# Kernel optimization log

Measured on AMD Instinct MI355X. Metric: run time of the kernel, lower is better.

Reference implementation:

```python
import jax, jax.numpy as jnp
import numpy as np

EMB = 128
HID = 512
B = 8192
W = 128


def setup_inputs() -> dict:
    key = jax.random.key(0)
    k1, k2, k3, k4, k5, k6, k7 = jax.random.split(key, 7)
    context_info = jax.random.normal(k1, (B, 4 * HID), dtype=jnp.float32)
    window = jax.random.normal(k2, (B, W, EMB), dtype=jnp.float32)
    window_mask = jax.random.bernoulli(k3, 0.9, (B, W))
    # guarantee at least one valid position per row (center is always valid)
    window_mask = window_mask.at[:, W // 2].set(True)
    ctr = jax.random.normal(k4, (B, EMB), dtype=jnp.float32)
    # learned params
    W_bilinear = jax.random.normal(k5, (EMB, EMB), dtype=jnp.float32) / np.sqrt(EMB)  # nn.Bilinear weight [1, emb, emb] squeezed
    W_linear = jax.random.normal(k6, (1, 4 * HID + EMB), dtype=jnp.float32) / np.sqrt(4 * HID + EMB)
    b_linear = jax.random.normal(k7, (1,), dtype=jnp.float32) * 0.01
    return {"context_info": context_info, "window": window, "window_mask": window_mask,
            "ctr": ctr, "W_bilinear": W_bilinear, "W_linear": W_linear, "b_linear": b_linear}


def reference(context_info, window, window_mask, ctr, W_bilinear, W_linear, b_linear):
    # bilinear attention score: ctr^T W window_t  -> [B, W]
    e = jnp.einsum('be,ef,bwf->bw', ctr, W_bilinear, window)
    invalid = jnp.logical_not(window_mask)
    e = jnp.where(invalid, -jnp.inf, e)
    # subtract per-row max (masked_fill of the broadcast max to 0 at invalid slots)
    m = jnp.max(e, axis=1, keepdims=True)            # [B, 1]
    e = e - jnp.where(invalid, 0.0, m)               # broadcast to [B, W]
    at_weights = jax.nn.softmax(e, axis=1)
    at_weights = jnp.where(invalid, 0.0, at_weights)
    # weighted sum over window -> [B, emb]
    context_eos = jnp.einsum('bw,bwe->be', at_weights, window)
    context_full = jnp.concatenate([context_info, context_eos], axis=1)
    logits = context_full @ W_linear.T + b_linear    # [B, 1]
    return logits
```

## Files before the change

kernel.cpp:

```cpp
#include <hip/hip_runtime.h>

#define EMB  128
#define HID4 2048
#define WIN  128

__global__ __launch_bounds__(256) void eos_fused_kernel(
    const float* __restrict__ ci,
    const float* __restrict__ window,
    const unsigned char* __restrict__ mask_raw,
    const float* __restrict__ ctr,
    const float* __restrict__ Wb,
    const float* __restrict__ WL,
    const float* __restrict__ bL,
    float* __restrict__ out)
{
    const int b    = blockIdx.x;
    const int tid  = threadIdx.x;
    const int lane = tid & 63;
    const int wave = tid >> 6;

    __shared__ float ctr_s[EMB];
    __shared__ float pu_s[2][EMB];
    __shared__ float u_s[EMB];
    __shared__ float acc_s[8][EMB];
    __shared__ float mz_s[8][2];
    __shared__ float red_s[4];
    __shared__ unsigned long long det_s[4][2];
    __shared__ int mode_s;

    {
        const unsigned int* mw = (const unsigned int*)mask_raw;
        int hi = 0, nf = 0;
        if (tid < 128) {
            unsigned int v = mw[tid];
            hi = (v & 0xFFFFFF00u) ? 1 : 0;
            nf = (v != 0u && v != 0x3F800000u) ? 1 : 0;
        }
        unsigned long long bh = __ballot(hi);
        unsigned long long bf = __ballot(nf);
        if (lane == 0) { det_s[wave][0] = bh; det_s[wave][1] = bf; }
    }
    if (tid < EMB) ctr_s[tid] = ctr[(size_t)b * EMB + tid];
    __syncthreads();
    if (tid == 0) {
        unsigned long long ah = det_s[0][0] | det_s[1][0] | det_s[2][0] | det_s[3][0];
        unsigned long long af = det_s[0][1] | det_s[1][1] | det_s[2][1] | det_s[3][1];
        mode_s = (af == 0ULL) ? 2 : (ah ? 0 : 1);
    }

    {
        const int f  = tid & (EMB - 1);
        const int h  = tid >> 7;
        const int e0 = h * 64;
        float s = 0.f;
        #pragma unroll 8
        for (int e = 0; e < 64; ++e)
            s = fmaf(ctr_s[e0 + e], Wb[(e0 + e) * EMB + f], s);
        pu_s[h][f] = s;
    }
    __syncthreads();
    if (tid < EMB) u_s[tid] = pu_s[0][tid] + pu_s[1][tid];
    __syncthreads();

    const int mode = mode_s;
    const int hl   = lane & 31;
    const int hw   = wave * 2 + (lane >> 5);
    float4 u4;
    u4.x = u_s[hl*4+0]; u4.y = u_s[hl*4+1]; u4.z = u_s[hl*4+2]; u4.w = u_s[hl*4+3];

    const float4*        win4 = (const float4*)(window + (size_t)b * WIN * EMB);
    const unsigned char* m8   = mask_raw + (size_t)b * WIN;
    const int*           m32  = (const int*)mask_raw + (size_t)b * WIN;
    const float*         mf   = (const float*)mask_raw + (size_t)b * WIN;

    float  m_run = -1e30f, Z = 0.f;
    float4 acc = make_float4(0.f, 0.f, 0.f, 0.f);

    #pragma unroll 4
    for (int i = 0; i < 16; ++i) {
        const int w = i * 8 + hw;
        float4 wv = win4[w * 32 + hl];
        bool valid;
        if (mode == 0)      valid = (m8[w]  != 0);
        else if (mode == 1) valid = (m32[w] != 0);
        else                valid = (mf[w]  != 0.0f);
        float s = wv.x * u4.x;
        s = fmaf(wv.y, u4.y, s);
        s = fmaf(wv.z, u4.z, s);
        s = fmaf(wv.w, u4.w, s);
        s += __shfl_xor(s, 1);
        s += __shfl_xor(s, 2);
        s += __shfl_xor(s, 4);
        s += __shfl_xor(s, 8);
        s += __shfl_xor(s, 16);
        const float m_new = valid ? fmaxf(m_run, s) : m_run;
        const float scale = __expf(m_run - m_new);
        const float p     = valid ? __expf(s - m_new) : 0.f;
        Z = fmaf(Z, scale, p);
        acc.x = fmaf(acc.x, scale, p * wv.x);
        acc.y = fmaf(acc.y, scale, p * wv.y);
        acc.z = fmaf(acc.z, scale, p * wv.z);
        acc.w = fmaf(acc.w, scale, p * wv.w);
        m_run = m_new;
    }

    acc_s[hw][hl*4+0] = acc.x;
    acc_s[hw][hl*4+1] = acc.y;
    acc_s[hw][hl*4+2] = acc.z;
    acc_s[hw][hl*4+3] = acc.w;
    if (hl == 0) { mz_s[hw][0] = m_run; mz_s[hw][1] = Z; }
    __syncthreads();

    float ce = 0.f;
    if (tid < EMB) {
        float M = mz_s[0][0];
        #pragma unroll
        for (int p = 1; p < 8; ++p) M = fmaxf(M, mz_s[p][0]);
        float Zt = 0.f, a = 0.f;
        #pragma unroll
        for (int p = 0; p < 8; ++p) {
            const float sc = __expf(mz_s[p][0] - M);
            Zt = fmaf(mz_s[p][1], sc, Zt);
            a  = fmaf(acc_s[p][tid], sc, a);
        }
        ce = a / Zt;
    }
    __syncthreads();
    if (tid < EMB) u_s[tid] = ce;
    __syncthreads();

    const float4* ci4 = (const float4*)(ci + (size_t)b * HID4);
    const float4* wl4 = (const float4*)WL;
    float part;
    {
        float4 c0 = ci4[tid],       w0 = wl4[tid];
        float4 c1 = ci4[tid + 256], w1 = wl4[tid + 256];
        part = c0.x * w0.x;
        part = fmaf(c0.y, w0.y, part);
        part = fmaf(c0.z, w0.z, part);
        part = fmaf(c0.w, w0.w, part);
        part = fmaf(c1.x, w1.x, part);
        part = fmaf(c1.y, w1.y, part);
        part = fmaf(c1.z, w1.z, part);
        part = fmaf(c1.w, w1.w, part);
    }
    if (tid < EMB) part = fmaf(u_s[tid], WL[HID4 + tid], part);

    part += __shfl_xor(part, 1);
    part += __shfl_xor(part, 2);
    part += __shfl_xor(part, 4);
    part += __shfl_xor(part, 8);
    part += __shfl_xor(part, 16);
    part += __shfl_xor(part, 32);
    if (lane == 0) red_s[wave] = part;
    __syncthreads();
    if (tid == 0)
        out[b] = red_s[0] + red_s[1] + red_s[2] + red_s[3] + bL[0];
}

extern "C" void kernel_launch(void* const* d_in, const int* in_sizes, int n_in,
                              void* d_out, int out_size, void* d_ws, size_t ws_size,
                              hipStream_t stream) {
    const float*         ci     = (const float*)d_in[0];
    const float*         window = (const float*)d_in[1];
    const unsigned char* mask   = (const unsigned char*)d_in[2];
    const float*         ctr    = (const float*)d_in[3];
    const float*         Wb     = (const float*)d_in[4];
    const float*         WL     = (const float*)d_in[5];
    const float*         bL     = (const float*)d_in[6];
    float*               out    = (float*)d_out;

    const int B = in_sizes[0] / HID4;
    hipLaunchKernelGGL(eos_fused_kernel, dim3(B), dim3(256), 0, stream,
                       ci, window, mask, ctr, Wb, WL, bL, out);
}
```

Before: 125.2 us.

## Preload window rows into registers and replace online softmax with two-pass

All 16 float4 window values per thread and the context_info/W_linear operands are loaded at kernel start, so the long global loads overlap the mask detection and the ctr·W_bilinear projection. The per-thread online softmax with rescaling is replaced by storing scores to shared memory, a block-wide max and sum reduction, then a plain weighted accumulation using the register-resident window. This removes the serial exp/rescale chain and the dependent load-use stalls, but raises register pressure (64 floats of window per thread) and adds extra barriers.

```diff
diff --git a/kernel.cpp b/kernel.cpp
--- a/kernel.cpp
+++ b/kernel.cpp
@@ -18,15 +18,30 @@
     const int tid  = threadIdx.x;
     const int lane = tid & 63;
     const int wave = tid >> 6;
+    const int hl   = lane & 31;
+    const int hw   = wave * 2 + (lane >> 5);
 
     __shared__ float ctr_s[EMB];
     __shared__ float pu_s[2][EMB];
     __shared__ float u_s[EMB];
+    __shared__ float s_s[WIN];
+    __shared__ float p_s[WIN];
     __shared__ float acc_s[8][EMB];
-    __shared__ float mz_s[8][2];
     __shared__ float red_s[4];
+    __shared__ float zinv_s;
     __shared__ unsigned long long det_s[4][2];
     __shared__ int mode_s;
+
+    const float4* win4 = (const float4*)(window + (size_t)b * WIN * EMB);
+    float4 wv[16];
+    #pragma unroll
+    for (int i = 0; i < 16; ++i)
+        wv[i] = win4[(i * 8 + hw) * 32 + hl];
+
+    const float4* ci4 = (const float4*)(ci + (size_t)b * HID4);
+    const float4* wl4 = (const float4*)WL;
+    float4 c0 = ci4[tid], c1 = ci4[tid + 256];
+    float4 w0 = wl4[tid], w1 = wl4[tid + 256];
 
     {
         const unsigned int* mw = (const unsigned int*)mask_raw;
@@ -48,6 +63,16 @@
         mode_s = (af == 0ULL) ? 2 : (ah ? 0 : 1);
     }
 
+    float part;
+    part = c0.x * w0.x;
+    part = fmaf(c0.y, w0.y, part);
+    part = fmaf(c0.z, w0.z, part);
+    part = fmaf(c0.w, w0.w, part);
+    part = fmaf(c1.x, w1.x, part);
+    part = fmaf(c1.y, w1.y, part);
+    part = fmaf(c1.z, w1.z, part);
+    part = fmaf(c1.w, w1.w, part);
+
     {
         const int f  = tid & (EMB - 1);
         const int h  = tid >> 7;
@@ -62,90 +87,80 @@
     if (tid < EMB) u_s[tid] = pu_s[0][tid] + pu_s[1][tid];
     __syncthreads();
 
-    const int mode = mode_s;
-    const int hl   = lane & 31;
-    const int hw   = wave * 2 + (lane >> 5);
     float4 u4;
     u4.x = u_s[hl*4+0]; u4.y = u_s[hl*4+1]; u4.z = u_s[hl*4+2]; u4.w = u_s[hl*4+3];
 
-    const float4*        win4 = (const float4*)(window + (size_t)b * WIN * EMB);
-    const unsigned char* m8   = mask_raw + (size_t)b * WIN;
-    const int*           m32  = (const int*)mask_raw + (size_t)b * WIN;
-    const float*         mf   = (const float*)mask_raw + (size_t)b * WIN;
-
-    float  m_run = -1e30f, Z = 0.f;
-    float4 acc = make_float4(0.f, 0.f, 0.f, 0.f);
-
-    #pragma unroll 4
+    #pragma unroll
     for (int i = 0; i < 16; ++i) {
-        const int w = i * 8 + hw;
-        float4 wv = win4[w * 32 + hl];
-        bool valid;
-        if (mode == 0)      valid = (m8[w]  != 0);
-        else if (mode == 1) valid = (m32[w] != 0);
-        else                valid = (mf[w]  != 0.0f);
-        float s = wv.x * u4.x;
-        s = fmaf(wv.y, u4.y, s);
-        s = fmaf(wv.z, u4.z, s);
-        s = fmaf(wv.w, u4.w, s);
+        float s = wv[i].x * u4.x;
+        s = fmaf(wv[i].y, u4.y, s);
+        s = fmaf(wv[i].z, u4.z, s);
+        s = fmaf(wv[i].w, u4.w, s);
         s += __shfl_xor(s, 1);
         s += __shfl_xor(s, 2);
         s += __shfl_xor(s, 4);
         s += __shfl_xor(s, 8);
         s += __shfl_xor(s, 16);
-        const float m_new = valid ? fmaxf(m_run, s) : m_run;
-        const float scale = __expf(m_run - m_new);
-        const float p     = valid ? __expf(s - m_new) : 0.f;
-        Z = fmaf(Z, scale, p);
-        acc.x = fmaf(acc.x, scale, p * wv.x);
-        acc.y = fmaf(acc.y, scale, p * wv.y);
-        acc.z = fmaf(acc.z, scale, p * wv.z);
-        acc.w = fmaf(acc.w, scale, p * wv.w);
-        m_run = m_new;
+        if (hl == 0) s_s[i * 8 + hw] = s;
     }
-
-    acc_s[hw][hl*4+0] = acc.x;
-    acc_s[hw][hl*4+1] = acc.y;
-    acc_s[hw][hl*4+2] = acc.z;
-    acc_s[hw][hl*4+3] = acc.w;
-    if (hl == 0) { mz_s[hw][0] = m_run; mz_s[hw][1] = Z; }
     __syncthreads();
 
-    float ce = 0.f;
-    if (tid < EMB) {
-        float M = mz_s[0][0];
-        #pragma unroll
-        for (int p = 1; p < 8; ++p) M = fmaxf(M, mz_s[p][0]);
-        float Zt = 0.f, a = 0.f;
-        #pragma unroll
-        for (int p = 0; p < 8; ++p) {
-            const float sc = __expf(mz_s[p][0] - M);
-            Zt = fmaf(mz_s[p][1], sc, Zt);
-            a  = fmaf(acc_s[p][tid], sc, a);
-        }
-        ce = a / Zt;
+    const int mode = mode_s;
+    bool  valid = false;
+    float sc    = 0.f;
+    if (tid < WIN) {
+        if (mode == 0)      valid = (mask_raw[(size_t)b * WIN + tid] != 0);
+        else if (mode == 1) valid = (((const int*)mask_raw)[(size_t)b * WIN + tid] != 0);
+        else                valid = (((const float*)mask_raw)[(size_t)b * WIN + tid] != 0.f);
+        sc = s_s[tid];
+        float sv = valid ? sc : -1e30f;
+        sv = fmaxf(sv, __shfl_xor(sv, 1));
+        sv = fmaxf(sv, __shfl_xor(sv, 2));
+        sv = fmaxf(sv, __shfl_xor(sv, 4));
+        sv = fmaxf(sv, __shfl_xor(sv, 8));
+        sv = fmaxf(sv, __shfl_xor(sv, 16));
+        sv = fmaxf(sv, __shfl_xor(sv, 32));
+        if (lane == 0) red_s[wave] = sv;
     }
     __syncthreads();
-    if (tid < EMB) u_s[tid] = ce;
+    if (tid < WIN) {
+        const float M = fmaxf(red_s[0], red_s[1]);
+        const float p = valid ? __expf(sc - M) : 0.f;
+        p_s[tid] = p;
+        float z = p;
+        z += __shfl_xor(z, 1);
+        z += __shfl_xor(z, 2);
+        z += __shfl_xor(z, 4);
+        z += __shfl_xor(z, 8);
+        z += __shfl_xor(z, 16);
+        z += __shfl_xor(z, 32);
+        if (lane == 0) red_s[2 + wave] = z;
+    }
+    __syncthreads();
+    if (tid == 0) zinv_s = 1.f / (red_s[2] + red_s[3]);
+
+    float4 a4 = make_float4(0.f, 0.f, 0.f, 0.f);
+    #pragma unroll
+    for (int i = 0; i < 16; ++i) {
+        const float p = p_s[i * 8 + hw];
+        a4.x = fmaf(p, wv[i].x, a4.x);
+        a4.y = fmaf(p, wv[i].y, a4.y);
+        a4.z = fmaf(p, wv[i].z, a4.z);
+        a4.w = fmaf(p, wv[i].w, a4.w);
+    }
+    acc_s[hw][hl*4+0] = a4.x;
+    acc_s[hw][hl*4+1] = a4.y;
+    acc_s[hw][hl*4+2] = a4.z;
+    acc_s[hw][hl*4+3] = a4.w;
     __syncthreads();
 
-    const float4* ci4 = (const float4*)(ci + (size_t)b * HID4);
-    const float4* wl4 = (const float4*)WL;
-    float part;
-    {
-        float4 c0 = ci4[tid],       w0 = wl4[tid];
-        float4 c1 = ci4[tid + 256], w1 = wl4[tid + 256];
-        part = c0.x * w0.x;
-        part = fmaf(c0.y, w0.y, part);
-        part = fmaf(c0.z, w0.z, part);
-        part = fmaf(c0.w, w0.w, part);
-        part = fmaf(c1.x, w1.x, part);
-        part = fmaf(c1.y, w1.y, part);
-        part = fmaf(c1.z, w1.z, part);
-        part = fmaf(c1.w, w1.w, part);
+    if (tid < EMB) {
+        float a = 0.f;
+        #pragma unroll
+        for (int p = 0; p < 8; ++p) a += acc_s[p][tid];
+        const float ce = a * zinv_s;
+        part = fmaf(ce, WL[HID4 + tid], part);
     }
-    if (tid < EMB) part = fmaf(u_s[tid], WL[HID4 + tid], part);
-
     part += __shfl_xor(part, 1);
     part += __shfl_xor(part, 2);
     part += __shfl_xor(part, 4);
```

New measurement: 168.7 us. 34.7% more time.
